# Performance work log

Hardware: AMD Instinct MI355X
Metric: run time of the kernel (lower is better)

## Reference

```python
import jax, jax.numpy as jnp
import numpy as np

N, D, L, H = 4, 512, 2048, 8  # batch, feat_dim, seq_len, num_heads


def setup_inputs() -> dict:
    key = jax.random.key(0)
    k1, k2, k3, k4 = jax.random.split(key, 4)
    x = jax.random.normal(k1, (N, D, L), dtype=jnp.float32)
    w_qkv = jax.random.normal(k2, (3 * D, D, 1), dtype=jnp.float32) * 0.02   # 1x1 conv
    w_dw = jax.random.normal(k3, (3 * D, 1, 3), dtype=jnp.float32) * 0.02    # depthwise k=3
    w_proj = jax.random.normal(k4, (D, D, 1), dtype=jnp.float32) * 0.02      # 1x1 conv
    temperature = jnp.ones((1, H, 1, 1), dtype=jnp.float32)
    return {"x": x, "w_qkv": w_qkv, "w_dw": w_dw, "w_proj": w_proj, "temperature": temperature}


def _conv1x1(x, w):
    # x: (n, c_in, l), w: (c_out, c_in, 1)
    return jnp.einsum('oc,ncl->nol', w[:, :, 0], x)


def _l2norm(t, eps=1e-12):
    # matches F.normalize: t / max(||t||_2, eps) along last dim
    n = jnp.sqrt(jnp.sum(t * t, axis=-1, keepdims=True))
    return t / jnp.maximum(n, eps)


def reference(x, w_qkv, w_dw, w_proj, temperature):
    n, d, l = x.shape
    h = temperature.shape[1]
    dh = d // h

    qkv = _conv1x1(x, w_qkv)                               # (n, 3d, l)
    qkv = jax.lax.conv_general_dilated(
        qkv, w_dw, window_strides=(1,), padding=[(1, 1)],
        dimension_numbers=('NCH', 'OIH', 'NCH'),
        feature_group_count=3 * d)                          # depthwise conv, (n, 3d, l)

    q, k, v = jnp.split(qkv, 3, axis=1)                     # each (n, d, l)
    # (n, d, l) -> (n, h, dh, l) -> (n, h, l, dh)
    q = q.reshape(n, h, dh, l).transpose(0, 1, 3, 2)
    k = k.reshape(n, h, dh, l).transpose(0, 1, 3, 2)
    v = v.reshape(n, h, dh, l).transpose(0, 1, 3, 2)

    q = _l2norm(q)
    k = _l2norm(k)

    scores = jnp.einsum('nhqd,nhkd->nhqk', q, k) * temperature  # (n, h, l, l)
    attn = jax.nn.softmax(scores, axis=-1)
    out = jnp.einsum('nhqk,nhkd->nhqd', attn, v)                # (n, h, l, dh)
    out = out.transpose(0, 1, 3, 2).reshape(n, d, l)            # (n, d, l)
    return _conv1x1(out, w_proj)
```

## Files before the change

### kernel.cpp

```cpp
#include <hip/hip_runtime.h>
#include <hip/hip_bf16.h>
#include <cstdint>
#include <cstddef>

#define N_B 4
#define D_F 512
#define L_S 2048
#define H_N 8
#define DH  64
#define C3  (3*D_F)

typedef __attribute__((ext_vector_type(8)))  short short8;
typedef __attribute__((ext_vector_type(4)))  float f32x4;
typedef __attribute__((ext_vector_type(16))) float f32x16;

__device__ __forceinline__ unsigned int pk_bf16(float a, float b) {
    __hip_bfloat162 h = __float22bfloat162_rn(float2{a, b});
    union { __hip_bfloat162 h; unsigned int u; } cv;
    cv.h = h;
    return cv.u;
}
__device__ __forceinline__ unsigned short bf16_rn(float f) {
    union { float f; unsigned int u; } c; c.f = f;
    unsigned int r = c.u + 0x7FFF + ((c.u >> 16) & 1);
    return (unsigned short)(r >> 16);
}
__device__ __forceinline__ float bf16_f(unsigned short h) {
    union { unsigned int u; float f; } c; c.u = ((unsigned int)h) << 16;
    return c.f;
}

__device__ __forceinline__ void gll16(const unsigned short* g, unsigned short* l) {
    __builtin_amdgcn_global_load_lds(
        (const __attribute__((address_space(1))) unsigned int*)g,
        (__attribute__((address_space(3))) unsigned int*)l,
        16, 0, 0);
}

__global__ __launch_bounds__(256) void cvt_split_w(const float* __restrict__ wq,
                                                   unsigned short* __restrict__ wq_hi,
                                                   unsigned short* __restrict__ wq_lo,
                                                   int n4q,
                                                   const float* __restrict__ wp,
                                                   unsigned short* __restrict__ wp_hi,
                                                   unsigned short* __restrict__ wp_lo,
                                                   int n4p) {
    int i = blockIdx.x * 256 + threadIdx.x;
    const float* src;
    unsigned short *hi, *lo;
    int idx;
    if (i < n4q) { src = wq; hi = wq_hi; lo = wq_lo; idx = i; }
    else if (i < n4q + n4p) { src = wp; hi = wp_hi; lo = wp_lo; idx = i - n4q; }
    else return;
    float4 v = ((const float4*)src)[idx];
    ushort4 h, l;
    h.x = bf16_rn(v.x); l.x = bf16_rn(v.x - bf16_f(h.x));
    h.y = bf16_rn(v.y); l.y = bf16_rn(v.y - bf16_f(h.y));
    h.z = bf16_rn(v.z); l.z = bf16_rn(v.z - bf16_f(h.z));
    h.w = bf16_rn(v.w); l.w = bf16_rn(v.w - bf16_f(h.w));
    ((ushort4*)hi)[idx] = h;
    ((ushort4*)lo)[idx] = l;
}

__global__ __launch_bounds__(256) void cvt_xT(const float* __restrict__ x,
                                              unsigned short* __restrict__ xT,
                                              int C) {
    __shared__ float tile[64][65];
    const int tid = threadIdx.x;
    const int l0  = blockIdx.x * 64;
    const int c0  = blockIdx.y * 64;
    const int n   = blockIdx.z;

    const float* xn = x + (size_t)n * C * L_S;
#pragma unroll
    for (int r = 0; r < 16; ++r) {
        int c = r * 4 + (tid >> 6);
        int l = tid & 63;
        tile[c][l] = xn[(size_t)(c0 + c) * L_S + l0 + l];
    }
    __syncthreads();

    unsigned short* xn_t = xT + (size_t)n * L_S * C;
#pragma unroll
    for (int r = 0; r < 8; ++r) {
        int l  = r * 8 + (tid >> 5);
        int cp = tid & 31;
        unsigned int pk = pk_bf16(tile[cp * 2][l], tile[cp * 2 + 1][l]);
        *(unsigned int*)&xn_t[(size_t)(l0 + l) * C + c0 + cp * 2] = pk;
    }
}

template<int SPLIT, int OUT_BF16>
__global__ __launch_bounds__(256) void gemm_mfma2(const unsigned short* __restrict__ Whi,
                                                  const unsigned short* __restrict__ Wlo,
                                                  const unsigned short* __restrict__ XThi,
                                                  const unsigned short* __restrict__ XTlo,
                                                  void* __restrict__ Y,
                                                  int O, int C) {
    __shared__ unsigned short Wt[SPLIT ? 2 : 1][4][128 * 8];
    __shared__ unsigned short Xt[SPLIT ? 2 : 1][4][128 * 8];

    const int tid  = threadIdx.x;
    const int lane = tid & 63;
    const int w    = tid >> 6;
    const int g    = lane >> 4;
    const int c    = lane & 15;
    const int wr   = (w >> 1) * 64;
    const int wc   = (w & 1) * 64;
    const int l0   = blockIdx.x * 128;
    const int o0   = blockIdx.y * 128;
    const int n    = blockIdx.z;

    const unsigned short* XTn_hi = XThi + (size_t)n * L_S * C;
    const unsigned short* XTn_lo = SPLIT ? (XTlo + (size_t)n * L_S * C) : nullptr;

    const int rhalf = (w & 1) * 64;
    const int cpA   = w >> 1;
    const int cpB   = 2 + (w >> 1);
    const size_t wrowA = (size_t)(o0 + rhalf + lane) * C;
    const size_t xrowA = (size_t)(l0 + rhalf + lane) * C;

    f32x4 acc[4][4];
#pragma unroll
    for (int mt = 0; mt < 4; ++mt)
#pragma unroll
        for (int nt = 0; nt < 4; ++nt) acc[mt][nt] = (f32x4){0.f, 0.f, 0.f, 0.f};

    for (int c0 = 0; c0 < C; c0 += 32) {
        __syncthreads();
        gll16(Whi + wrowA + c0 + cpA * 8, &Wt[0][cpA][rhalf * 8]);
        gll16(Whi + wrowA + c0 + cpB * 8, &Wt[0][cpB][rhalf * 8]);
        gll16(XTn_hi + xrowA + c0 + cpA * 8, &Xt[0][cpA][rhalf * 8]);
        gll16(XTn_hi + xrowA + c0 + cpB * 8, &Xt[0][cpB][rhalf * 8]);
        if (SPLIT) {
            gll16(Wlo + wrowA + c0 + cpA * 8, &Wt[1][cpA][rhalf * 8]);
            gll16(Wlo + wrowA + c0 + cpB * 8, &Wt[1][cpB][rhalf * 8]);
            gll16(XTn_lo + xrowA + c0 + cpA * 8, &Xt[1][cpA][rhalf * 8]);
            gll16(XTn_lo + xrowA + c0 + cpB * 8, &Xt[1][cpB][rhalf * 8]);
        }
        __syncthreads();

        short8 a0[4], b0[4];
#pragma unroll
        for (int mt = 0; mt < 4; ++mt) a0[mt] = *(short8*)&Wt[0][g][(wr + mt * 16 + c) * 8];
#pragma unroll
        for (int nt = 0; nt < 4; ++nt) b0[nt] = *(short8*)&Xt[0][g][(wc + nt * 16 + c) * 8];

        if (SPLIT) {
            short8 a1[4], b1[4];
#pragma unroll
            for (int mt = 0; mt < 4; ++mt) a1[mt] = *(short8*)&Wt[1][g][(wr + mt * 16 + c) * 8];
#pragma unroll
            for (int nt = 0; nt < 4; ++nt) b1[nt] = *(short8*)&Xt[1][g][(wc + nt * 16 + c) * 8];
#pragma unroll
            for (int mt = 0; mt < 4; ++mt)
#pragma unroll
                for (int nt = 0; nt < 4; ++nt) {
                    acc[mt][nt] = __builtin_amdgcn_mfma_f32_16x16x32_bf16(a0[mt], b0[nt], acc[mt][nt], 0, 0, 0);
                    acc[mt][nt] = __builtin_amdgcn_mfma_f32_16x16x32_bf16(a0[mt], b1[nt], acc[mt][nt], 0, 0, 0);
                    acc[mt][nt] = __builtin_amdgcn_mfma_f32_16x16x32_bf16(a1[mt], b0[nt], acc[mt][nt], 0, 0, 0);
                }
        } else {
#pragma unroll
            for (int mt = 0; mt < 4; ++mt)
#pragma unroll
                for (int nt = 0; nt < 4; ++nt)
                    acc[mt][nt] = __builtin_amdgcn_mfma_f32_16x16x32_bf16(a0[mt], b0[nt], acc[mt][nt], 0, 0, 0);
        }
    }

#pragma unroll
    for (int mt = 0; mt < 4; ++mt) {
#pragma unroll
        for (int r = 0; r < 4; ++r) {
            int oo = o0 + wr + mt * 16 + g * 4 + r;
            size_t rowbase = ((size_t)n * O + oo) * L_S;
#pragma unroll
            for (int nt = 0; nt < 4; ++nt) {
                int ll = l0 + wc + nt * 16 + c;
                if (OUT_BF16)
                    ((unsigned short*)Y)[rowbase + ll] = bf16_rn(acc[mt][nt][r]);
                else
                    ((float*)Y)[rowbase + ll] = acc[mt][nt][r];
            }
        }
    }
}

__global__ __launch_bounds__(256) void fused_qk2(const unsigned short* __restrict__ qkv_bf,
                                                 const float* __restrict__ w_dw,
                                                 unsigned short* __restrict__ Qb,
                                                 unsigned short* __restrict__ Kb) {
    __shared__ unsigned short rows[64 * 264];
    __shared__ float wsm[192];
    const int tid = threadIdx.x;
    const int l0  = blockIdx.x * 256;
    const int gg  = blockIdx.y;
    const int n   = blockIdx.z;
    const int head = gg & 7;
    const int ch0  = (gg < 8) ? head * 64 : 512 + head * 64;

    if (tid < 192) wsm[tid] = w_dw[ch0 * 3 + tid];

    const unsigned short* base = qkv_bf + ((size_t)n * C3 + ch0) * L_S;
    for (int f = tid; f < 2048; f += 256) {
        int e = f >> 5, s = f & 31;
        *(uint4*)&rows[e * 264 + s * 8] = *(const uint4*)&base[(size_t)e * L_S + l0 + s * 8];
    }
    if (tid < 64) {
        rows[tid * 264 + 256] = (l0 > 0) ? base[(size_t)tid * L_S + l0 - 1] : (unsigned short)0;
    } else if (tid < 128) {
        int e = tid - 64;
        rows[e * 264 + 257] = (l0 + 256 < L_S) ? base[(size_t)e * L_S + l0 + 256] : (unsigned short)0;
    }
    __syncthreads();

    const int lL = tid;
    const int iL = (lL == 0)   ? 256 : lL - 1;
    const int iR = (lL == 255) ? 257 : lL + 1;
    float y[64];
    float s = 0.f;
#pragma unroll
    for (int e = 0; e < 64; ++e) {
        float a = bf16_f(rows[e * 264 + iL]);
        float b = bf16_f(rows[e * 264 + lL]);
        float d = bf16_f(rows[e * 264 + iR]);
        float v = wsm[e * 3 + 0] * a + wsm[e * 3 + 1] * b + wsm[e * 3 + 2] * d;
        y[e] = v;
        s += v * v;
    }
    float sc = 1.0f / fmaxf(sqrtf(s), 1e-12f);

    const int l = l0 + tid;
    unsigned short* dst = ((gg < 8) ? Qb : Kb) + (size_t)(n * H_N + head) * 8 * L_S * 8;
#pragma unroll
    for (int p = 0; p < 8; ++p) {
        uint4 pk = make_uint4(pk_bf16(y[8 * p + 0] * sc, y[8 * p + 1] * sc),
                              pk_bf16(y[8 * p + 2] * sc, y[8 * p + 3] * sc),
                              pk_bf16(y[8 * p + 4] * sc, y[8 * p + 5] * sc),
                              pk_bf16(y[8 * p + 6] * sc, y[8 * p + 7] * sc));
        *(uint4*)&dst[((size_t)p * L_S + l) * 8] = pk;
    }
}

__global__ __launch_bounds__(256) void fused_v2(const unsigned short* __restrict__ qkv_bf,
                                                const float* __restrict__ w_dw,
                                                unsigned short* __restrict__ Vb) {
    const int tid = threadIdx.x;
    const int e   = tid & 63;
    const int jp  = blockIdx.x * 4 + (tid >> 6);
    const int h   = blockIdx.y;
    const int n   = blockIdx.z;
    const int ch  = 1024 + h * 64 + e;
    const unsigned short* row = qkv_bf + ((size_t)n * C3 + ch) * L_S;
    const int k0 = jp * 8;

    uint4 mv = *(const uint4*)&row[k0];
    unsigned int lw = (jp > 0)   ? *(const unsigned int*)&row[k0 - 2] : 0u;
    unsigned int rw = (jp < 255) ? *(const unsigned int*)&row[k0 + 8] : 0u;

    float v[10];
    v[0] = bf16_f((unsigned short)(lw >> 16));
    v[1] = bf16_f((unsigned short)(mv.x & 0xFFFF));
    v[2] = bf16_f((unsigned short)(mv.x >> 16));
    v[3] = bf16_f((unsigned short)(mv.y & 0xFFFF));
    v[4] = bf16_f((unsigned short)(mv.y >> 16));
    v[5] = bf16_f((unsigned short)(mv.z & 0xFFFF));
    v[6] = bf16_f((unsigned short)(mv.z >> 16));
    v[7] = bf16_f((unsigned short)(mv.w & 0xFFFF));
    v[8] = bf16_f((unsigned short)(mv.w >> 16));
    v[9] = bf16_f((unsigned short)(rw & 0xFFFF));

    float w0 = w_dw[ch * 3 + 0], w1 = w_dw[ch * 3 + 1], w2 = w_dw[ch * 3 + 2];
    unsigned int o[4];
#pragma unroll
    for (int i = 0; i < 4; ++i) {
        float y0 = w0 * v[2 * i + 0] + w1 * v[2 * i + 1] + w2 * v[2 * i + 2];
        float y1 = w0 * v[2 * i + 1] + w1 * v[2 * i + 2] + w2 * v[2 * i + 3];
        o[i] = pk_bf16(y0, y1);
    }
    uint4 ov = make_uint4(o[0], o[1], o[2], o[3]);
    *(uint4*)&Vb[(((size_t)(n * H_N + h) * 256 + jp) * 512) + e * 8] = ov;
}

__global__ __launch_bounds__(512, 2) void attn11(const unsigned short* __restrict__ Qb,
                                                 const unsigned short* __restrict__ Kb,
                                                 const unsigned short* __restrict__ Vb,
                                                 const float* __restrict__ temp,
                                                 unsigned short* __restrict__ aoT_hi,
                                                 unsigned short* __restrict__ aoT_lo) {
    __shared__ float Ot[128 * 64];
    __shared__ float smB[128];
    __shared__ float smA[128];

    const int tid  = threadIdx.x;
    const int lane = tid & 63;
    const int w    = tid >> 6;
    const int g2   = w >> 2;
    const int wv   = w & 3;
    const int c32  = lane & 31;
    const int h    = lane >> 5;
    const int q0   = blockIdx.x * 128;
    const int hd   = blockIdx.y;
    const int n    = blockIdx.z;

    const size_t hb = (size_t)(n * H_N + hd);
    const unsigned short* Qh = Qb + hb * 8 * L_S * 8;
    const unsigned short* Kh = Kb + hb * 8 * L_S * 8;
    const unsigned short* Vh = Vb + hb * 256 * 512;
    const float t    = temp[hd];
    const float negm = -fabsf(t);

    bool dirA;
    {
        auto tp = __builtin_amdgcn_permlane32_swap((int)lane, (int)(lane + 64), false, false);
        unsigned xv = (unsigned)tp[0];
        bool ok = (lane < 32) ? true : (xv == (unsigned)(lane + 32));
        dirA = (__ballot(ok) == 0xFFFFFFFFFFFFFFFFull);
    }

    short8 qa[4];
#pragma unroll
    for (int es = 0; es < 4; ++es)
        qa[es] = *(const short8*)&Qh[((size_t)(es * 2 + h) * L_S + q0 + wv * 32 + c32) * 8];

    f32x16 acc0, acc1;
#pragma unroll
    for (int i = 0; i < 16; ++i) { acc0[i] = 0.f; acc1[i] = 0.f; }
    float sumP = 0.f;

    for (int it = 0; it < 16; ++it) {
        const int k0 = (it * 2 + g2) * 64;

        f32x16 sf0, sf1;
#pragma unroll
        for (int i = 0; i < 16; ++i) { sf0[i] = 0.f; sf1[i] = 0.f; }
        short8 ka0[4], ka1[4];
#pragma unroll
        for (int es = 0; es < 4; ++es) {
            const unsigned short* krow = Kh + (size_t)(es * 2 + h) * L_S * 8;
            ka0[es] = *(const short8*)&krow[(k0 + c32) * 8];
            ka1[es] = *(const short8*)&krow[(k0 + 32 + c32) * 8];
        }
        __builtin_amdgcn_s_setprio(1);
#pragma unroll
        for (int es = 0; es < 4; ++es) {
            sf0 = __builtin_amdgcn_mfma_f32_32x32x16_bf16(ka0[es], qa[es], sf0, 0, 0, 0);
            sf1 = __builtin_amdgcn_mfma_f32_32x32x16_bf16(ka1[es], qa[es], sf1, 0, 0, 0);
        }
        __builtin_amdgcn_s_setprio(0);

        short8 pa[4];
        {
            unsigned int W_[16];
#pragma unroll
            for (int G = 0; G < 4; ++G) {
                float p0 = __expf(fmaf(sf0[4*G+0], t, negm));
                float p1 = __expf(fmaf(sf0[4*G+1], t, negm));
                float p2 = __expf(fmaf(sf0[4*G+2], t, negm));
                float p3 = __expf(fmaf(sf0[4*G+3], t, negm));
                sumP += (p0 + p1) + (p2 + p3);
                W_[2*G]   = pk_bf16(p0, p1);
                W_[2*G+1] = pk_bf16(p2, p3);
                float u0 = __expf(fmaf(sf1[4*G+0], t, negm));
                float u1 = __expf(fmaf(sf1[4*G+1], t, negm));
                float u2 = __expf(fmaf(sf1[4*G+2], t, negm));
                float u3 = __expf(fmaf(sf1[4*G+3], t, negm));
                sumP += (u0 + u1) + (u2 + u3);
                W_[8+2*G]   = pk_bf16(u0, u1);
                W_[8+2*G+1] = pk_bf16(u2, u3);
            }
#pragma unroll
            for (int ks = 0; ks < 4; ++ks) {
                unsigned w0 = dirA ? W_[4*ks]   : W_[4*ks+2];
                unsigned w2 = dirA ? W_[4*ks+2] : W_[4*ks];
                unsigned w1 = dirA ? W_[4*ks+1] : W_[4*ks+3];
                unsigned w3 = dirA ? W_[4*ks+3] : W_[4*ks+1];
                auto r02 = __builtin_amdgcn_permlane32_swap((int)w0, (int)w2, false, false);
                auto r13 = __builtin_amdgcn_permlane32_swap((int)w1, (int)w3, false, false);
                unsigned a0 = dirA ? (unsigned)r02[0] : (unsigned)r02[1];
                unsigned a2 = dirA ? (unsigned)r02[1] : (unsigned)r02[0];
                unsigned a1 = dirA ? (unsigned)r13[0] : (unsigned)r13[1];
                unsigned a3 = dirA ? (unsigned)r13[1] : (unsigned)r13[0];
                uint4 pu = make_uint4(a0, a1, a2, a3);
                pa[ks] = *(short8*)&pu;
            }
        }

        __builtin_amdgcn_s_setprio(1);
#pragma unroll
        for (int ks = 0; ks < 4; ++ks) {
            const unsigned short* vrow = Vh + (size_t)((k0 >> 3) + ks * 2 + h) * 512;
            short8 vb0 = *(const short8*)&vrow[c32 * 8];
            short8 vb1 = *(const short8*)&vrow[(32 + c32) * 8];
            acc0 = __builtin_amdgcn_mfma_f32_32x32x16_bf16(pa[ks], vb0, acc0, 0, 0, 0);
            acc1 = __builtin_amdgcn_mfma_f32_32x32x16_bf16(pa[ks], vb1, acc1, 0, 0, 0);
        }
        __builtin_amdgcn_s_setprio(0);
    }

    sumP += __shfl_xor(sumP, 32);

    if (g2 == 1) {
        smB[wv * 32 + c32] = sumP;
#pragma unroll
        for (int r = 0; r < 16; ++r) {
            int ql = (r & 3) + 8 * (r >> 2) + 4 * h;
            int qg = wv * 32 + ql;
            Ot[qg * 64 + c32]      = acc0[r];
            Ot[qg * 64 + 32 + c32] = acc1[r];
        }
    } else {
        smA[wv * 32 + c32] = sumP;
    }
    __syncthreads();

    if (g2 == 0) {
        float b0[16], b1[16], inv[16];
#pragma unroll
        for (int r = 0; r < 16; ++r) {
            int ql = (r & 3) + 8 * (r >> 2) + 4 * h;
            int qg = wv * 32 + ql;
            b0[r] = Ot[qg * 64 + c32];
            b1[r] = Ot[qg * 64 + 32 + c32];
            inv[r] = 1.0f / (smA[qg] + smB[qg]);
        }
#pragma unroll
        for (int r = 0; r < 16; ++r) {
            int ql = (r & 3) + 8 * (r >> 2) + 4 * h;
            int qg = wv * 32 + ql;
            Ot[qg * 64 + (c32 ^ (qg & 31))]        = (acc0[r] + b0[r]) * inv[r];
            Ot[qg * 64 + ((32 + c32) ^ (qg & 31))] = (acc1[r] + b1[r]) * inv[r];
        }
    }
    __syncthreads();

    for (int tt = tid; tt < 8192; tt += 512) {
        int qq = tt >> 6, e = tt & 63;
        float v = Ot[qq * 64 + (e ^ (qq & 31))];
        unsigned short hi_ = bf16_rn(v);
        unsigned short lo_ = bf16_rn(v - bf16_f(hi_));
        size_t off = ((size_t)n * L_S + q0 + qq) * D_F + hd * 64 + e;
        aoT_hi[off] = hi_;
        aoT_lo[off] = lo_;
    }
}

extern "C" void kernel_launch(void* const* d_in, const int* in_sizes, int n_in,
                              void* d_out, int out_size, void* d_ws, size_t ws_size,
                              hipStream_t stream) {
    const float* x      = (const float*)d_in[0];
    const float* w_qkv  = (const float*)d_in[1];
    const float* w_dw   = (const float*)d_in[2];
    const float* w_proj = (const float*)d_in[3];
    const float* temp   = (const float*)d_in[4];
    float* out = (float*)d_out;

    const size_t WQE = (size_t)C3 * D_F;
    const size_t WPE = (size_t)D_F * D_F;

    char* ws = (char*)d_ws;
    unsigned short* qkv_bf = (unsigned short*)ws;
    unsigned short* Qb     = (unsigned short*)(ws + 25165824);
    unsigned short* Kb     = (unsigned short*)(ws + 33554432);
    unsigned short* Vb     = (unsigned short*)(ws + 41943040);
    unsigned short* xT     = (unsigned short*)(ws + 50331648);
    unsigned short* aoT_lo = (unsigned short*)(ws + 58720256);
    unsigned short* wq_hi  = (unsigned short*)(ws + 67108864);
    unsigned short* wq_lo  = wq_hi + WQE;
    unsigned short* wp_hi  = (unsigned short*)(ws + 70254592);
    unsigned short* wp_lo  = wp_hi + WPE;
    unsigned short* aoT_hi = xT;

    cvt_xT<<<dim3(L_S / 64, D_F / 64, N_B), 256, 0, stream>>>(x, xT, D_F);
    {
        int n4q = (int)(WQE / 4), n4p = (int)(WPE / 4);
        cvt_split_w<<<dim3((n4q + n4p + 255) / 256), 256, 0, stream>>>(
            w_qkv, wq_hi, wq_lo, n4q, w_proj, wp_hi, wp_lo, n4p);
    }

    gemm_mfma2<0, 1><<<dim3(L_S / 128, C3 / 128, N_B), 256, 0, stream>>>(
        wq_hi, nullptr, xT, nullptr, qkv_bf, C3, D_F);

    fused_qk2<<<dim3(L_S / 256, 16, N_B), 256, 0, stream>>>(qkv_bf, w_dw, Qb, Kb);
    fused_v2<<<dim3(64, H_N, N_B), 256, 0, stream>>>(qkv_bf, w_dw, Vb);

    attn11<<<dim3(L_S / 128, H_N, N_B), 512, 0, stream>>>(Qb, Kb, Vb, temp, aoT_hi, aoT_lo);

    gemm_mfma2<1, 0><<<dim3(L_S / 128, D_F / 128, N_B), 256, 0, stream>>>(
        wp_hi, wp_lo, aoT_hi, aoT_lo, out, D_F, D_F);
}
```

Before: 155.6 us.

## Fold temperature into Q, use exp2, compute softmax row sums via MFMA

Q is prescaled during normalization by temperature times log2(e), so the attention loop needs only an add and a native exp2 per score instead of an fma and expf. The per-lane scalar row-sum accumulation is replaced by an extra MFMA that multiplies the bf16 probabilities by a ones vector, which also makes the sum match the bf16-rounded P used for the output. This removes VALU work from the softmax hot loop but adds an extra MFMA per k-step and another 16-register accumulator, which may raise register pressure at two blocks per SM.

Measured after the change: 175.6 us. 12.9% more time.

```diff
diff --git a/kernel.cpp b/kernel.cpp
--- a/kernel.cpp
+++ b/kernel.cpp
@@ -13,6 +13,12 @@
 typedef __attribute__((ext_vector_type(8)))  short short8;
 typedef __attribute__((ext_vector_type(4)))  float f32x4;
 typedef __attribute__((ext_vector_type(16))) float f32x16;
+
+#if __has_builtin(__builtin_amdgcn_exp2f)
+#define EXP2F(x) __builtin_amdgcn_exp2f(x)
+#else
+#define EXP2F(x) __expf((x) * 0.6931471805599453f)
+#endif
 
 __device__ __forceinline__ unsigned int pk_bf16(float a, float b) {
     __hip_bfloat162 h = __float22bfloat162_rn(float2{a, b});
@@ -189,6 +195,7 @@
 
 __global__ __launch_bounds__(256) void fused_qk2(const unsigned short* __restrict__ qkv_bf,
                                                  const float* __restrict__ w_dw,
+                                                 const float* __restrict__ temp,
                                                  unsigned short* __restrict__ Qb,
                                                  unsigned short* __restrict__ Kb) {
     __shared__ unsigned short rows[64 * 264];
@@ -230,6 +237,7 @@
         s += v * v;
     }
     float sc = 1.0f / fmaxf(sqrtf(s), 1e-12f);
+    if (gg < 8) sc *= temp[head] * 1.44269504088896f;
 
     const int l = l0 + tid;
     unsigned short* dst = ((gg < 8) ? Qb : Kb) + (size_t)(n * H_N + head) * 8 * L_S * 8;
@@ -283,7 +291,7 @@
     *(uint4*)&Vb[(((size_t)(n * H_N + h) * 256 + jp) * 512) + e * 8] = ov;
 }
 
-__global__ __launch_bounds__(512, 2) void attn11(const unsigned short* __restrict__ Qb,
+__global__ __launch_bounds__(512, 2) void attn12(const unsigned short* __restrict__ Qb,
                                                  const unsigned short* __restrict__ Kb,
                                                  const unsigned short* __restrict__ Vb,
                                                  const float* __restrict__ temp,
@@ -291,7 +299,6 @@
                                                  unsigned short* __restrict__ aoT_lo) {
     __shared__ float Ot[128 * 64];
     __shared__ float smB[128];
-    __shared__ float smA[128];
 
     const int tid  = threadIdx.x;
     const int lane = tid & 63;
@@ -308,8 +315,8 @@
     const unsigned short* Qh = Qb + hb * 8 * L_S * 8;
     const unsigned short* Kh = Kb + hb * 8 * L_S * 8;
     const unsigned short* Vh = Vb + hb * 256 * 512;
-    const float t    = temp[hd];
-    const float negm = -fabsf(t);
+    const float t2    = temp[hd] * 1.44269504088896f;
+    const float negm2 = -fabsf(t2);
 
     bool dirA;
     {
@@ -319,15 +326,18 @@
         dirA = (__ballot(ok) == 0xFFFFFFFFFFFFFFFFull);
     }
 
+    short8 ones8;
+#pragma unroll
+    for (int i = 0; i < 8; ++i) ones8[i] = (short)0x3F80;
+
     short8 qa[4];
 #pragma unroll
     for (int es = 0; es < 4; ++es)
         qa[es] = *(const short8*)&Qh[((size_t)(es * 2 + h) * L_S + q0 + wv * 32 + c32) * 8];
 
-    f32x16 acc0, acc1;
-#pragma unroll
-    for (int i = 0; i < 16; ++i) { acc0[i] = 0.f; acc1[i] = 0.f; }
-    float sumP = 0.f;
+    f32x16 acc0, acc1, acc_s;
+#pragma unroll
+    for (int i = 0; i < 16; ++i) { acc0[i] = 0.f; acc1[i] = 0.f; acc_s[i] = 0.f; }
 
     for (int it = 0; it < 16; ++it) {
         const int k0 = (it * 2 + g2) * 64;
@@ -355,18 +365,16 @@
             unsigned int W_[16];
 #pragma unroll
             for (int G = 0; G < 4; ++G) {
-                float p0 = __expf(fmaf(sf0[4*G+0], t, negm));
-                float p1 = __expf(fmaf(sf0[4*G+1], t, negm));
-                float p2 = __expf(fmaf(sf0[4*G+2], t, negm));
-                float p3 = __expf(fmaf(sf0[4*G+3], t, negm));
-                sumP += (p0 + p1) + (p2 + p3);
+                float p0 = EXP2F(sf0[4*G+0] + negm2);
+                float p1 = EXP2F(sf0[4*G+1] + negm2);
+                float p2 = EXP2F(sf0[4*G+2] + negm2);
+                float p3 = EXP2F(sf0[4*G+3] + negm2);
                 W_[2*G]   = pk_bf16(p0, p1);
                 W_[2*G+1] = pk_bf16(p2, p3);
-                float u0 = __expf(fmaf(sf1[4*G+0], t, negm));
-                float u1 = __expf(fmaf(sf1[4*G+1], t, negm));
-                float u2 = __expf(fmaf(sf1[4*G+2], t, negm));
-                float u3 = __expf(fmaf(sf1[4*G+3], t, negm));
-                sumP += (u0 + u1) + (u2 + u3);
+                float u0 = EXP2F(sf1[4*G+0] + negm2);
+                float u1 = EXP2F(sf1[4*G+1] + negm2);
+                float u2 = EXP2F(sf1[4*G+2] + negm2);
+                float u3 = EXP2F(sf1[4*G+3] + negm2);
                 W_[8+2*G]   = pk_bf16(u0, u1);
                 W_[8+2*G+1] = pk_bf16(u2, u3);
             }
@@ -393,16 +401,21 @@
             const unsigned short* vrow = Vh + (size_t)((k0 >> 3) + ks * 2 + h) * 512;
             short8 vb0 = *(const short8*)&vrow[c32 * 8];
             short8 vb1 = *(const short8*)&vrow[(32 + c32) * 8];
-            acc0 = __builtin_amdgcn_mfma_f32_32x32x16_bf16(pa[ks], vb0, acc0, 0, 0, 0);
-            acc1 = __builtin_amdgcn_mfma_f32_32x32x16_bf16(pa[ks], vb1, acc1, 0, 0, 0);
+            acc0  = __builtin_amdgcn_mfma_f32_32x32x16_bf16(pa[ks], vb0,   acc0,  0, 0, 0);
+            acc1  = __builtin_amdgcn_mfma_f32_32x32x16_bf16(pa[ks], vb1,   acc1,  0, 0, 0);
+            acc_s = __builtin_amdgcn_mfma_f32_32x32x16_bf16(pa[ks], ones8, acc_s, 0, 0, 0);
         }
         __builtin_amdgcn_s_setprio(0);
     }
 
-    sumP += __shfl_xor(sumP, 32);
-
     if (g2 == 1) {
-        smB[wv * 32 + c32] = sumP;
+        if (c32 == 0) {
+#pragma unroll
+            for (int r = 0; r < 16; ++r) {
+                int ql = (r & 3) + 8 * (r >> 2) + 4 * h;
+                smB[wv * 32 + ql] = acc_s[r];
+            }
+        }
 #pragma unroll
         for (int r = 0; r < 16; ++r) {
             int ql = (r & 3) + 8 * (r >> 2) + 4 * h;
@@ -410,8 +423,6 @@
             Ot[qg * 64 + c32]      = acc0[r];
             Ot[qg * 64 + 32 + c32] = acc1[r];
         }
-    } else {
-        smA[wv * 32 + c32] = sumP;
     }
     __syncthreads();
 
@@ -423,7 +434,7 @@
             int qg = wv * 32 + ql;
             b0[r] = Ot[qg * 64 + c32];
             b1[r] = Ot[qg * 64 + 32 + c32];
-            inv[r] = 1.0f / (smA[qg] + smB[qg]);
+            inv[r] = 1.0f / (acc_s[r] + smB[qg]);
         }
 #pragma unroll
         for (int r = 0; r < 16; ++r) {
@@ -482,10 +493,10 @@
     gemm_mfma2<0, 1><<<dim3(L_S / 128, C3 / 128, N_B), 256, 0, stream>>>(
         wq_hi, nullptr, xT, nullptr, qkv_bf, C3, D_F);
 
-    fused_qk2<<<dim3(L_S / 256, 16, N_B), 256, 0, stream>>>(qkv_bf, w_dw, Qb, Kb);
+    fused_qk2<<<dim3(L_S / 256, 16, N_B), 256, 0, stream>>>(qkv_bf, w_dw, temp, Qb, Kb);
     fused_v2<<<dim3(64, H_N, N_B), 256, 0, stream>>>(qkv_bf, w_dw, Vb);
 
-    attn11<<<dim3(L_S / 128, H_N, N_B), 512, 0, stream>>>(Qb, Kb, Vb, temp, aoT_hi, aoT_lo);
+    attn12<<<dim3(L_S / 128, H_N, N_B), 512, 0, stream>>>(Qb, Kb, Vb, temp, aoT_hi, aoT_lo);
 
     gemm_mfma2<1, 0><<<dim3(L_S / 128, D_F / 128, N_B), 256, 0, stream>>>(
         wp_hi, wp_lo, aoT_hi, aoT_lo, out, D_F, D_F);
```
